# Optimization experiments

Measured on AMD Instinct MI355X. Metric: run time of the kernel, lower is better.

Reference implementation:

```python
import jax, jax.numpy as jnp
import numpy as np

NH, KD, VD, C = 8, 64, 64, 256

def conv1x1(x, w, b):
    # x: (B,C,D,H,W), w: (O,C), b: (O,)
    return jnp.einsum('bcdhw,oc->bodhw', x, w) + b[None, :, None, None, None]

def setup_inputs() -> dict:
    key = jax.random.key(0)
    ks = jax.random.split(key, 8)
    B, D, H, W = 2, 32, 32, 32
    s = 0.02
    return {
        'x': jax.random.normal(ks[0], (B, C, D, H, W), jnp.float32),
        'q_w': jax.random.normal(ks[1], (NH * KD, C), jnp.float32) * s,
        'q_b': jnp.zeros((NH * KD,), jnp.float32),
        'kv_w': jax.random.normal(ks[2], (KD + VD, C), jnp.float32) * s,
        'kv_b': jnp.zeros((KD + VD,), jnp.float32),
        'proj_w': jax.random.normal(ks[3], (C, NH * VD), jnp.float32) * s,
        'proj_b': jnp.zeros((C,), jnp.float32),
        'layer_scale': jnp.full((C, 1, 1, 1), 1e-5, jnp.float32),
    }

def reference(x, q_w, q_b, kv_w, kv_b, proj_w, proj_b, layer_scale):
    B, Cc, D, H, W = x.shape
    scale = VD ** -0.5
    # q: (B, nh, D, H, W, kd) -> flatten(3,5) -> (B, nh, D, H*W*kd)
    q = conv1x1(x, q_w, q_b).reshape(B, NH, KD, D, H, W).transpose(0, 1, 3, 4, 5, 2)
    q = q.reshape(B, NH, D, H * W * KD)
    kv = conv1x1(x, kv_w, kv_b)  # (B, kd+vd, D, H, W)
    k = kv[:, :KD].transpose(0, 2, 3, 4, 1).reshape(B, D, H * W * KD)  # shared across heads
    v = kv[:, KD:].transpose(0, 2, 3, 4, 1).reshape(B, D, H * W * VD)
    attn = jax.nn.softmax(jnp.einsum('bnqf,bkf->bnqk', q, k) * scale, axis=-1)  # (B,nh,D,D)
    o = jnp.einsum('bnqk,bkf->bnqf', attn, v)  # (B, nh, D, H*W*vd)
    # transpose(1,2) then row-major reshape, exactly as torch
    o = o.transpose(0, 2, 1, 3).reshape(B, D, H, W, NH * VD).transpose(0, 4, 1, 2, 3)
    out = conv1x1(o, proj_w, proj_b)
    return out * layer_scale[None]
```

## Files before the change

### kernel.cpp

```cpp
#include <hip/hip_runtime.h>
#include <math.h>

#define SS 32768
#define FQL_LDS_BYTES 149504

typedef _Float16 half4v __attribute__((ext_vector_type(4)));
typedef _Float16 half8v __attribute__((ext_vector_type(8)));
typedef float float4v __attribute__((ext_vector_type(4)));

__device__ __forceinline__ void gload16(const void* g, void* l) {
    __builtin_amdgcn_global_load_lds(
        (const __attribute__((address_space(1))) unsigned int*)g,
        (__attribute__((address_space(3))) unsigned int*)l, 16, 0, 0);
}

__global__ __launch_bounds__(256)
void cvt_x_kernel(const float* __restrict__ x, _Float16* __restrict__ x_t)
{
    __shared__ float ls[64][65];
    const int b = blockIdx.z, c0 = blockIdx.y * 64, s0 = blockIdx.x * 64;
    const int t = threadIdx.x;
    const int tr = t >> 4, tc = t & 15;
#pragma unroll
    for (int p = 0; p < 4; p++) {
        int c_l = p * 16 + tr;
        float4v v = *(const float4v*)(x + (size_t)(b * 256 + c0 + c_l) * SS + s0 + tc * 4);
        ls[c_l][tc * 4 + 0] = v.x;
        ls[c_l][tc * 4 + 1] = v.y;
        ls[c_l][tc * 4 + 2] = v.z;
        ls[c_l][tc * 4 + 3] = v.w;
    }
    __syncthreads();
#pragma unroll
    for (int p = 0; p < 4; p++) {
        int s_l = p * 16 + tr;
        half4v h;
        h.x = (_Float16)ls[tc * 4 + 0][s_l];
        h.y = (_Float16)ls[tc * 4 + 1][s_l];
        h.z = (_Float16)ls[tc * 4 + 2][s_l];
        h.w = (_Float16)ls[tc * 4 + 3][s_l];
        *(half4v*)(x_t + ((size_t)b * SS + s0 + s_l) * 256 + c0 + tc * 4) = h;
    }
}

__global__ __launch_bounds__(256)
void cvt_w3_kernel(const float* __restrict__ s0, _Float16* __restrict__ d0,
                   const float* __restrict__ s1, _Float16* __restrict__ d1,
                   const float* __restrict__ s2, _Float16* __restrict__ d2)
{
    int bx = blockIdx.x;
    if (bx < 128) {
        int idx = (bx * 256 + threadIdx.x) * 4;
        int e = idx & 7;
        int lane = (idx >> 3) & 63;
        int l15 = lane & 15, lq = lane >> 4;
        int blk = idx >> 9;
        int i = blk & 3, ks = (blk >> 2) & 7, nh = blk >> 5;
        const float* src = s0 + (size_t)(nh * 64 + i * 16 + l15) * 256 + ks * 32 + lq * 8 + e;
        float4v v = *(const float4v*)src;
        half4v hh;
        hh.x = (_Float16)v.x; hh.y = (_Float16)v.y; hh.z = (_Float16)v.z; hh.w = (_Float16)v.w;
        *(half4v*)(d0 + idx) = hh;
    } else {
        const float* s; _Float16* d; int base;
        if (bx < 160) { s = s1; d = d1; base = bx - 128; }
        else          { s = s2; d = d2; base = bx - 160; }
        int i = (base * 256 + threadIdx.x) * 4;
        float4v v = *(const float4v*)(s + i);
        half4v hh;
        hh.x = (_Float16)v.x; hh.y = (_Float16)v.y; hh.z = (_Float16)v.z; hh.w = (_Float16)v.w;
        *(half4v*)(d + i) = hh;
    }
}

__global__ __launch_bounds__(256)
void convkv_kernel(const _Float16* __restrict__ x_t,
                   const _Float16* __restrict__ wkv,
                   const float* __restrict__ kv_b,
                   _Float16* __restrict__ kv_t)
{
    __shared__ _Float16 smem[128 * 136];
    _Float16* const Ws = smem;
    _Float16* const Xs = smem + 128 * 64;
    const int b = blockIdx.y;
    const int s0 = blockIdx.x * 128;
    const int t = threadIdx.x;
    const int w = t >> 6, l = t & 63;
    const int om = (w & 1) * 64, sn = (w >> 1) * 64;

    const int lr = l >> 3;
    const int gch = ((l & 7) - lr) & 7;
    const int m15 = l & 15;
    const int sl0 = ((((l >> 4) + (l & 7)) & 7)) * 8;
    const int sl1 = ((((l >> 4) + 4 + (l & 7)) & 7)) * 8;

    float4v acc[4][4];
#pragma unroll
    for (int i = 0; i < 4; i++)
#pragma unroll
        for (int j = 0; j < 4; j++) acc[i][j] = (float4v){0.f, 0.f, 0.f, 0.f};

    const _Float16* wg = wkv + (size_t)(32 * w + lr) * 256 + gch * 8;
    const _Float16* xg = x_t + ((size_t)b * SS + s0 + 32 * w + lr) * 256 + gch * 8;
    _Float16* wl = &Ws[(32 * w) * 64];
    _Float16* xl = &Xs[(32 * w) * 64];

    for (int c0 = 0; c0 < 256; c0 += 64) {
#pragma unroll
        for (int rb = 0; rb < 4; rb++) {
            gload16(wg + (size_t)rb * 8 * 256 + c0, wl + rb * 8 * 64);
            gload16(xg + (size_t)rb * 8 * 256 + c0, xl + rb * 8 * 64);
        }
        __syncthreads();
#pragma unroll
        for (int ks = 0; ks < 2; ks++) {
            const int sl = ks ? sl1 : sl0;
            half8v a[4], bb[4];
#pragma unroll
            for (int i = 0; i < 4; i++)
                a[i] = *(const half8v*)&Ws[(om + i * 16 + m15) * 64 + sl];
#pragma unroll
            for (int j = 0; j < 4; j++)
                bb[j] = *(const half8v*)&Xs[(sn + j * 16 + m15) * 64 + sl];
#pragma unroll
            for (int i = 0; i < 4; i++)
#pragma unroll
                for (int j = 0; j < 4; j++)
                    acc[i][j] = __builtin_amdgcn_mfma_f32_16x16x32_f16(a[i], bb[j], acc[i][j], 0, 0, 0);
        }
        __syncthreads();
    }
    const int qd = l >> 4, m = l & 15;
#pragma unroll
    for (int i = 0; i < 4; i++) {
        float bv[4];
#pragma unroll
        for (int r = 0; r < 4; r++) bv[r] = kv_b[om + i * 16 + qd * 4 + r];
#pragma unroll
        for (int j = 0; j < 4; j++) {
            half4v h;
            h.x = (_Float16)(acc[i][j].x + bv[0]);
            h.y = (_Float16)(acc[i][j].y + bv[1]);
            h.z = (_Float16)(acc[i][j].z + bv[2]);
            h.w = (_Float16)(acc[i][j].w + bv[3]);
            int s_l = sn + j * 16 + m;
            *(half4v*)&smem[s_l * 136 + om + i * 16 + qd * 4] = h;
        }
    }
    __syncthreads();
    const int sr = t >> 4, kk = t & 15;
#pragma unroll
    for (int p = 0; p < 8; p++) {
        int s_l = p * 16 + sr;
        half8v h8 = *(const half8v*)&smem[s_l * 136 + kk * 8];
        *(half8v*)(kv_t + ((size_t)b * SS + s0 + s_l) * 128 + kk * 8) = h8;
    }
}

__global__ __launch_bounds__(512)
void fq_logits_kernel(const _Float16* __restrict__ x_t,
                      const _Float16* __restrict__ wq_f,
                      const float* __restrict__ q_b,
                      const _Float16* __restrict__ kv_t,
                      float* __restrict__ Lpart)
{
    extern __shared__ _Float16 sm[];
    _Float16* const Xs = sm;
    _Float16* const Qs = sm + 32768;
    float* const scr = (float*)(sm + 65536);

    const int chunk = blockIdx.x, b = blockIdx.y;
    const int hw0 = chunk * 4;
    const int t = threadIdx.x;
    const int w = t >> 6, l = t & 63;
    const int l15 = l & 15, lq = l >> 4;
    const int h = w >> 1;
    const int ns = w & 1;
    const int n0 = ns * 64;

#pragma unroll
    for (int ii = 0; ii < 8; ii++) {
        int r = w * 16 + ii * 2 + (l >> 5);
        int p = l & 31;
        int sc = (p - 4 * r) & 31;
        int qd = r >> 2, hwl = r & 3;
        gload16(x_t + ((size_t)b * SS + qd * 1024 + hw0 + hwl) * 256 + sc * 8,
                Xs + (w * 16 + ii * 2) * 256);
    }

    half8v bk[8];
#pragma unroll
    for (int j = 0; j < 2; j++)
#pragma unroll
        for (int ksp = 0; ksp < 4; ksp++) {
            int kk = (ns * 4 + ksp) * 32 + lq * 8;
            bk[j * 4 + ksp] = *(const half8v*)(kv_t +
                ((size_t)b * SS + (size_t)(j * 16 + l15) * 1024 + hw0 + (kk >> 6)) * 128 + (kk & 63));
        }
    __syncthreads();

    _Float16* const Qs_h = Qs + h * 8192;
    float* const scr_h = scr + h * (32 * 36);
    float* const lp_g = Lpart + (((size_t)chunk * 2 + b) * 8) * 1024;

    for (int g = 0; g < 2; g++) {
        const int nh = g * 4 + h;
        const _Float16* wf = wq_f + ((size_t)nh * 32) * 512 + (size_t)l * 8;
        half8v aF[4], aN[4];
#pragma unroll
        for (int i = 0; i < 4; i++) aF[i] = *(const half8v*)(wf + (size_t)i * 512);
        float4v acc[4][4];
#pragma unroll
        for (int i = 0; i < 4; i++)
#pragma unroll
            for (int j = 0; j < 4; j++) acc[i][j] = (float4v){0.f, 0.f, 0.f, 0.f};
#pragma unroll
        for (int ks = 0; ks < 8; ks++) {
            if (ks < 7) {
#pragma unroll
                for (int i = 0; i < 4; i++)
                    aN[i] = *(const half8v*)(wf + (size_t)((ks + 1) * 4 + i) * 512);
            }
            const int p8 = (((ks * 4 + lq) + 4 * (l15 & 7)) & 31) * 8;
            half8v bF[4];
#pragma unroll
            for (int j = 0; j < 4; j++)
                bF[j] = *(const half8v*)&Xs[(n0 + j * 16 + l15) * 256 + p8];
#pragma unroll
            for (int i = 0; i < 4; i++)
#pragma unroll
                for (int j = 0; j < 4; j++)
                    acc[i][j] = __builtin_amdgcn_mfma_f32_16x16x32_f16(aF[i], bF[j], acc[i][j], 0, 0, 0);
#pragma unroll
            for (int i = 0; i < 4; i++) aF[i] = aN[i];
        }
#pragma unroll
        for (int i = 0; i < 4; i++) {
            int kb = i * 16 + lq * 4;
            float4v bv = *(const float4v*)(q_b + nh * 64 + kb);
#pragma unroll
            for (int j = 0; j < 4; j++) {
                int sp = n0 + j * 16 + l15;
                int key = ((sp ^ (sp >> 2)) & 7) << 3;
                half4v hv;
                hv.x = (_Float16)(acc[i][j].x + bv.x);
                hv.y = (_Float16)(acc[i][j].y + bv.y);
                hv.z = (_Float16)(acc[i][j].z + bv.z);
                hv.w = (_Float16)(acc[i][j].w + bv.w);
                *(half4v*)&Qs_h[sp * 64 + (kb ^ key)] = hv;
            }
        }
        __syncthreads();
        float4v lacc[2][2];
#pragma unroll
        for (int i = 0; i < 2; i++)
#pragma unroll
            for (int j = 0; j < 2; j++) lacc[i][j] = (float4v){0.f, 0.f, 0.f, 0.f};
#pragma unroll
        for (int ksp = 0; ksp < 4; ksp++) {
            int kk = (ns * 4 + ksp) * 32 + lq * 8;
            half8v a0, a1;
            {
                int sp = l15 * 4 + (kk >> 6);
                int key = ((sp ^ (sp >> 2)) & 7) << 3;
                a0 = *(const half8v*)&Qs_h[sp * 64 + ((kk & 63) ^ key)];
            }
            {
                int sp = (16 + l15) * 4 + (kk >> 6);
                int key = ((sp ^ (sp >> 2)) & 7) << 3;
                a1 = *(const half8v*)&Qs_h[sp * 64 + ((kk & 63) ^ key)];
            }
            lacc[0][0] = __builtin_amdgcn_mfma_f32_16x16x32_f16(a0, bk[ksp],     lacc[0][0], 0, 0, 0);
            lacc[0][1] = __builtin_amdgcn_mfma_f32_16x16x32_f16(a0, bk[4 + ksp], lacc[0][1], 0, 0, 0);
            lacc[1][0] = __builtin_amdgcn_mfma_f32_16x16x32_f16(a1, bk[ksp],     lacc[1][0], 0, 0, 0);
            lacc[1][1] = __builtin_amdgcn_mfma_f32_16x16x32_f16(a1, bk[4 + ksp], lacc[1][1], 0, 0, 0);
        }
        if (ns == 1) {
#pragma unroll
            for (int i = 0; i < 2; i++)
#pragma unroll
                for (int j = 0; j < 2; j++)
                    *(float4v*)&scr_h[(j * 16 + l15) * 36 + i * 16 + lq * 4] = lacc[i][j];
        }
        __syncthreads();
        if (ns == 0) {
            float* dst = lp_g + (size_t)nh * 1024;
#pragma unroll
            for (int i = 0; i < 2; i++)
#pragma unroll
                for (int j = 0; j < 2; j++) {
                    float4v o = lacc[i][j];
                    float4v p4 = *(const float4v*)&scr_h[(j * 16 + l15) * 36 + i * 16 + lq * 4];
                    o += p4;
                    int rb = i * 16 + lq * 4;
#pragma unroll
                    for (int rr = 0; rr < 4; rr++)
                        dst[(rb + rr) * 32 + j * 16 + l15] = o[rr];
                }
        }
    }
}

__global__ __launch_bounds__(256)
void softmax_kernel(const float* __restrict__ Lpart, float* __restrict__ Lsm)
{
    __shared__ float red[32][8][32];
    const int t = threadIdx.x;
    const int rl = t & 7, cs = t >> 3;
    const int row = blockIdx.x * 8 + rl;
    const int b = row >> 8, nh = (row >> 5) & 7, qd = row & 31;
    float4v p[8];
#pragma unroll
    for (int j4 = 0; j4 < 8; j4++) p[j4] = (float4v){0.f, 0.f, 0.f, 0.f};
    for (int cc = 0; cc < 8; cc++) {
        int chunk = cs + cc * 32;
        const float* src = Lpart + (((size_t)chunk * 2 + b) * 8 + nh) * 1024 + qd * 32;
#pragma unroll
        for (int j4 = 0; j4 < 8; j4++) p[j4] += *(const float4v*)(src + j4 * 4);
    }
#pragma unroll
    for (int j4 = 0; j4 < 8; j4++) *(float4v*)&red[cs][rl][j4 * 4] = p[j4];
    __syncthreads();
    const int r2 = t >> 5, j = t & 31;
    float s = 0.f;
#pragma unroll
    for (int c2 = 0; c2 < 32; c2++) s += red[c2][r2][j];
    float mx = s;
#pragma unroll
    for (int off = 16; off >= 1; off >>= 1) mx = fmaxf(mx, __shfl_xor(mx, off, 32));
    float e = expf((s - mx) * 0.125f);
    float sum = e;
#pragma unroll
    for (int off = 16; off >= 1; off >>= 1) sum += __shfl_xor(sum, off, 32);
    Lsm[(size_t)(blockIdx.x * 8 + r2) * 32 + j] = e / sum;
}

__global__ __launch_bounds__(256)
void attn_v_kernel(const _Float16* __restrict__ kv_t,
                   const float* __restrict__ attn,
                   _Float16* __restrict__ o_t)
{
    __shared__ float as_[2048];
    const int wq = blockIdx.x, hl = blockIdx.y;
    const int b = blockIdx.z >> 2, rc = blockIdx.z & 3;
    const int t = threadIdx.x;
    {
        const float* src = attn + (size_t)b * 8192 + rc * 2048;
#pragma unroll
        for (int ll = 0; ll < 2; ll++) {
            int idx = (t + ll * 256) * 4;
            *(float4v*)(&as_[idx]) = *(const float4v*)(src + idx);
        }
    }
    __syncthreads();
    const int q4 = t & 127;
    const int half = t >> 7;
    const int tt = q4 >> 4;
    const int vd = (q4 * 4) & 63;
    const int hw = hl * 256 + wq * 8 + tt;
    float4v vreg[32];
#pragma unroll
    for (int j = 0; j < 32; j++) {
        half4v hv = *(const half4v*)(kv_t + ((size_t)((b * 32 + j) * 1024 + hw)) * 128 + 64 + vd);
        vreg[j] = (float4v){(float)hv.x, (float)hv.y, (float)hv.z, (float)hv.w};
    }
    _Float16* outb = o_t + (size_t)b * SS * 512;
#pragma unroll 2
    for (int rr = 0; rr < 32; rr++) {
        int row_l = half * 32 + rr;
        int row = rc * 64 + row_l;
        int hh = row >> 5, d = row & 31;
        const float* arow = &as_[row_l * 32];
        float ax = 0.f, ay = 0.f, az = 0.f, aw = 0.f;
#pragma unroll
        for (int j4 = 0; j4 < 8; j4++) {
            float4v a4 = *(const float4v*)(&arow[j4 * 4]);
            float4v v0 = vreg[j4 * 4 + 0];
            float4v v1 = vreg[j4 * 4 + 1];
            float4v v2 = vreg[j4 * 4 + 2];
            float4v v3 = vreg[j4 * 4 + 3];
            ax = fmaf(a4.x, v0.x, ax); ay = fmaf(a4.x, v0.y, ay);
            az = fmaf(a4.x, v0.z, az); aw = fmaf(a4.x, v0.w, aw);
            ax = fmaf(a4.y, v1.x, ax); ay = fmaf(a4.y, v1.y, ay);
            az = fmaf(a4.y, v1.z, az); aw = fmaf(a4.y, v1.w, aw);
            ax = fmaf(a4.z, v2.x, ax); ay = fmaf(a4.z, v2.y, ay);
            az = fmaf(a4.z, v2.z, az); aw = fmaf(a4.z, v2.w, aw);
            ax = fmaf(a4.w, v3.x, ax); ay = fmaf(a4.w, v3.y, ay);
            az = fmaf(a4.w, v3.z, az); aw = fmaf(a4.w, v3.w, aw);
        }
        int hp = hh * 4 + hl;
        size_t sp = (size_t)d * 1024 + hp * 32 + wq;
        half4v o4;
        o4.x = (_Float16)ax; o4.y = (_Float16)ay; o4.z = (_Float16)az; o4.w = (_Float16)aw;
        *(half4v*)(outb + sp * 512 + q4 * 4) = o4;
    }
}

__global__ __launch_bounds__(256)
void proj_mfma_kernel(const _Float16* __restrict__ o_t,
                      const _Float16* __restrict__ wp,
                      const float* __restrict__ pb,
                      const float* __restrict__ ls,
                      float* __restrict__ out)
{
    __shared__ _Float16 Ws[128 * 64];
    __shared__ _Float16 Xs[128 * 64];
    const int b = blockIdx.y;
    const int bx = blockIdx.x;
    const int grp = bx >> 4, rem = bx & 15;
    const int s_tile = grp * 8 + (rem & 7);
    const int o_tile = rem >> 3;
    const int s0 = s_tile * 128, o0 = o_tile * 128;
    const int t = threadIdx.x;
    const int w = t >> 6, l = t & 63;
    const int om = (w & 1) * 64, sn = (w >> 1) * 64;

    const int lr = l >> 3;
    const int gch = ((l & 7) - lr) & 7;
    const int m15 = l & 15;
    const int sl0 = ((((l >> 4) + (l & 7)) & 7)) * 8;
    const int sl1 = ((((l >> 4) + 4 + (l & 7)) & 7)) * 8;

    float4v acc[4][4];
#pragma unroll
    for (int i = 0; i < 4; i++)
#pragma unroll
        for (int j = 0; j < 4; j++) acc[i][j] = (float4v){0.f, 0.f, 0.f, 0.f};

    const _Float16* wg = wp + (size_t)(o0 + 32 * w + lr) * 512 + gch * 8;
    const _Float16* xg = o_t + ((size_t)b * SS + s0 + 32 * w + lr) * 512 + gch * 8;
    _Float16* wl = &Ws[(32 * w) * 64];
    _Float16* xl = &Xs[(32 * w) * 64];

    for (int c0 = 0; c0 < 512; c0 += 64) {
#pragma unroll
        for (int rb = 0; rb < 4; rb++) {
            gload16(wg + (size_t)rb * 8 * 512 + c0, wl + rb * 8 * 64);
            gload16(xg + (size_t)rb * 8 * 512 + c0, xl + rb * 8 * 64);
        }
        __syncthreads();
#pragma unroll
        for (int ks = 0; ks < 2; ks++) {
            const int sl = ks ? sl1 : sl0;
            half8v a[4], bb[4];
#pragma unroll
            for (int i = 0; i < 4; i++)
                a[i] = *(const half8v*)&Ws[(om + i * 16 + m15) * 64 + sl];
#pragma unroll
            for (int j = 0; j < 4; j++)
                bb[j] = *(const half8v*)&Xs[(sn + j * 16 + m15) * 64 + sl];
#pragma unroll
            for (int i = 0; i < 4; i++)
#pragma unroll
                for (int j = 0; j < 4; j++)
                    acc[i][j] = __builtin_amdgcn_mfma_f32_16x16x32_f16(a[i], bb[j], acc[i][j], 0, 0, 0);
        }
        __syncthreads();
    }
    const int qd = l >> 4, m = l & 15;
#pragma unroll
    for (int i = 0; i < 4; i++) {
        float pbv[4], lsv[4];
#pragma unroll
        for (int r = 0; r < 4; r++) {
            int o = o0 + om + i * 16 + qd * 4 + r;
            pbv[r] = pb[o];
            lsv[r] = ls[o];
        }
#pragma unroll
        for (int j = 0; j < 4; j++) {
            int s = s0 + sn + j * 16 + m;
#pragma unroll
            for (int r = 0; r < 4; r++) {
                int o = o0 + om + i * 16 + qd * 4 + r;
                out[((size_t)b * 256 + o) * SS + s] = (acc[i][j][r] + pbv[r]) * lsv[r];
            }
        }
    }
}

extern "C" void kernel_launch(void* const* d_in, const int* in_sizes, int n_in,
                              void* d_out, int out_size, void* d_ws, size_t ws_size,
                              hipStream_t stream)
{
    const float* x      = (const float*)d_in[0];
    const float* q_w    = (const float*)d_in[1];
    const float* q_b    = (const float*)d_in[2];
    const float* kv_w   = (const float*)d_in[3];
    const float* kv_b   = (const float*)d_in[4];
    const float* proj_w = (const float*)d_in[5];
    const float* proj_b = (const float*)d_in[6];
    const float* ls     = (const float*)d_in[7];
    float* out = (float*)d_out;

    char* ws = (char*)d_ws;
    _Float16* x_t  = (_Float16*)(ws);
    _Float16* o_t  = (_Float16*)(ws + 33554432);
    float*    Lpart= (float*)   (ws + 33554432);
    _Float16* kv_t = (_Float16*)(ws + 100663296);
    float*    Lsm  = (float*)   (ws + 117440512);
    _Float16* wq_f = (_Float16*)(ws + 117506048);
    _Float16* wkv  = (_Float16*)(ws + 117768192);
    _Float16* wp   = (_Float16*)(ws + 117833728);

    static bool fql_attr_set = false;
    if (!fql_attr_set) {
        hipFuncSetAttribute(reinterpret_cast<const void*>(fq_logits_kernel),
                            hipFuncAttributeMaxDynamicSharedMemorySize, FQL_LDS_BYTES);
        fql_attr_set = true;
    }

    cvt_x_kernel<<<dim3(512, 4, 2), 256, 0, stream>>>(x, x_t);
    cvt_w3_kernel<<<dim3(288), 256, 0, stream>>>(q_w, wq_f, kv_w, wkv, proj_w, wp);

    convkv_kernel<<<dim3(256, 2), 256, 0, stream>>>(x_t, wkv, kv_b, kv_t);
    fq_logits_kernel<<<dim3(256, 2), 512, FQL_LDS_BYTES, stream>>>(x_t, wq_f, q_b, kv_t, Lpart);
    softmax_kernel<<<dim3(64), 256, 0, stream>>>(Lpart, Lsm);
    attn_v_kernel<<<dim3(32, 4, 8), 256, 0, stream>>>(kv_t, Lsm, o_t);
    proj_mfma_kernel<<<dim3(512, 2), 256, 0, stream>>>(o_t, wp, proj_b, ls, out);
}
```

Measured before the change: 242.1 us.

## Fuse KV 1x1 conv into fused Q-logits kernel, computing K/V from LDS-resident x tile

Removes the separate convkv kernel. The fq_logits kernel now computes K and V for its own 128 spatial positions from the x tile already in LDS, keeps K in LDS for the logits and writes only V to global memory for the attn_v stage. The weight conversion for kv_w moves to the fragment-packed layout used for q_w. The logits reduction is reorganised so each wave covers all 256 K-steps for half the rows, which drops the cross-wave scratch reduction. In exchange the fused kernel does more work per block and needs an extra sync and LDS region reuse.

```diff
diff --git a/kernel.cpp b/kernel.cpp
--- a/kernel.cpp
+++ b/kernel.cpp
@@ -2,7 +2,7 @@
 #include <math.h>
 
 #define SS 32768
-#define FQL_LDS_BYTES 149504
+#define FQL_LDS_BYTES 147456
 
 typedef _Float16 half4v __attribute__((ext_vector_type(4)));
 typedef _Float16 half8v __attribute__((ext_vector_type(8)));
@@ -49,111 +49,27 @@
                    const float* __restrict__ s2, _Float16* __restrict__ d2)
 {
     int bx = blockIdx.x;
-    if (bx < 128) {
-        int idx = (bx * 256 + threadIdx.x) * 4;
+    if (bx < 160) {
+        const float* s; _Float16* d; int base;
+        if (bx < 128) { s = s0; d = d0; base = bx; }
+        else          { s = s1; d = d1; base = bx - 128; }
+        int idx = (base * 256 + threadIdx.x) * 4;
         int e = idx & 7;
         int lane = (idx >> 3) & 63;
         int l15 = lane & 15, lq = lane >> 4;
         int blk = idx >> 9;
-        int i = blk & 3, ks = (blk >> 2) & 7, nh = blk >> 5;
-        const float* src = s0 + (size_t)(nh * 64 + i * 16 + l15) * 256 + ks * 32 + lq * 8 + e;
+        int i = blk & 3, ks = (blk >> 2) & 7, slab = blk >> 5;
+        const float* src = s + (size_t)(slab * 64 + i * 16 + l15) * 256 + ks * 32 + lq * 8 + e;
         float4v v = *(const float4v*)src;
         half4v hh;
         hh.x = (_Float16)v.x; hh.y = (_Float16)v.y; hh.z = (_Float16)v.z; hh.w = (_Float16)v.w;
-        *(half4v*)(d0 + idx) = hh;
+        *(half4v*)(d + idx) = hh;
     } else {
-        const float* s; _Float16* d; int base;
-        if (bx < 160) { s = s1; d = d1; base = bx - 128; }
-        else          { s = s2; d = d2; base = bx - 160; }
-        int i = (base * 256 + threadIdx.x) * 4;
-        float4v v = *(const float4v*)(s + i);
+        int i = ((bx - 160) * 256 + threadIdx.x) * 4;
+        float4v v = *(const float4v*)(s2 + i);
         half4v hh;
         hh.x = (_Float16)v.x; hh.y = (_Float16)v.y; hh.z = (_Float16)v.z; hh.w = (_Float16)v.w;
-        *(half4v*)(d + i) = hh;
-    }
-}
-
-__global__ __launch_bounds__(256)
-void convkv_kernel(const _Float16* __restrict__ x_t,
-                   const _Float16* __restrict__ wkv,
-                   const float* __restrict__ kv_b,
-                   _Float16* __restrict__ kv_t)
-{
-    __shared__ _Float16 smem[128 * 136];
-    _Float16* const Ws = smem;
-    _Float16* const Xs = smem + 128 * 64;
-    const int b = blockIdx.y;
-    const int s0 = blockIdx.x * 128;
-    const int t = threadIdx.x;
-    const int w = t >> 6, l = t & 63;
-    const int om = (w & 1) * 64, sn = (w >> 1) * 64;
-
-    const int lr = l >> 3;
-    const int gch = ((l & 7) - lr) & 7;
-    const int m15 = l & 15;
-    const int sl0 = ((((l >> 4) + (l & 7)) & 7)) * 8;
-    const int sl1 = ((((l >> 4) + 4 + (l & 7)) & 7)) * 8;
-
-    float4v acc[4][4];
-#pragma unroll
-    for (int i = 0; i < 4; i++)
-#pragma unroll
-        for (int j = 0; j < 4; j++) acc[i][j] = (float4v){0.f, 0.f, 0.f, 0.f};
-
-    const _Float16* wg = wkv + (size_t)(32 * w + lr) * 256 + gch * 8;
-    const _Float16* xg = x_t + ((size_t)b * SS + s0 + 32 * w + lr) * 256 + gch * 8;
-    _Float16* wl = &Ws[(32 * w) * 64];
-    _Float16* xl = &Xs[(32 * w) * 64];
-
-    for (int c0 = 0; c0 < 256; c0 += 64) {
-#pragma unroll
-        for (int rb = 0; rb < 4; rb++) {
-            gload16(wg + (size_t)rb * 8 * 256 + c0, wl + rb * 8 * 64);
-            gload16(xg + (size_t)rb * 8 * 256 + c0, xl + rb * 8 * 64);
-        }
-        __syncthreads();
-#pragma unroll
-        for (int ks = 0; ks < 2; ks++) {
-            const int sl = ks ? sl1 : sl0;
-            half8v a[4], bb[4];
-#pragma unroll
-            for (int i = 0; i < 4; i++)
-                a[i] = *(const half8v*)&Ws[(om + i * 16 + m15) * 64 + sl];
-#pragma unroll
-            for (int j = 0; j < 4; j++)
-                bb[j] = *(const half8v*)&Xs[(sn + j * 16 + m15) * 64 + sl];
-#pragma unroll
-            for (int i = 0; i < 4; i++)
-#pragma unroll
-                for (int j = 0; j < 4; j++)
-                    acc[i][j] = __builtin_amdgcn_mfma_f32_16x16x32_f16(a[i], bb[j], acc[i][j], 0, 0, 0);
-        }
-        __syncthreads();
-    }
-    const int qd = l >> 4, m = l & 15;
-#pragma unroll
-    for (int i = 0; i < 4; i++) {
-        float bv[4];
-#pragma unroll
-        for (int r = 0; r < 4; r++) bv[r] = kv_b[om + i * 16 + qd * 4 + r];
-#pragma unroll
-        for (int j = 0; j < 4; j++) {
-            half4v h;
-            h.x = (_Float16)(acc[i][j].x + bv[0]);
-            h.y = (_Float16)(acc[i][j].y + bv[1]);
-            h.z = (_Float16)(acc[i][j].z + bv[2]);
-            h.w = (_Float16)(acc[i][j].w + bv[3]);
-            int s_l = sn + j * 16 + m;
-            *(half4v*)&smem[s_l * 136 + om + i * 16 + qd * 4] = h;
-        }
-    }
-    __syncthreads();
-    const int sr = t >> 4, kk = t & 15;
-#pragma unroll
-    for (int p = 0; p < 8; p++) {
-        int s_l = p * 16 + sr;
-        half8v h8 = *(const half8v*)&smem[s_l * 136 + kk * 8];
-        *(half8v*)(kv_t + ((size_t)b * SS + s0 + s_l) * 128 + kk * 8) = h8;
+        *(half4v*)(d2 + i) = hh;
     }
 }
 
@@ -161,22 +77,22 @@
 void fq_logits_kernel(const _Float16* __restrict__ x_t,
                       const _Float16* __restrict__ wq_f,
                       const float* __restrict__ q_b,
-                      const _Float16* __restrict__ kv_t,
+                      const _Float16* __restrict__ wkv_f,
+                      const float* __restrict__ kv_b,
+                      _Float16* __restrict__ kv_t,
                       float* __restrict__ Lpart)
 {
     extern __shared__ _Float16 sm[];
-    _Float16* const Xs = sm;
-    _Float16* const Qs = sm + 32768;
-    float* const scr = (float*)(sm + 65536);
+    _Float16* const Xs  = sm;
+    _Float16* const Qs  = sm + 32768;
+    _Float16* const Vst = sm + 32768;
+    _Float16* const Ks  = sm + 65536;
 
     const int chunk = blockIdx.x, b = blockIdx.y;
     const int hw0 = chunk * 4;
     const int t = threadIdx.x;
     const int w = t >> 6, l = t & 63;
     const int l15 = l & 15, lq = l >> 4;
-    const int h = w >> 1;
-    const int ns = w & 1;
-    const int n0 = ns * 64;
 
 #pragma unroll
     for (int ii = 0; ii < 8; ii++) {
@@ -187,20 +103,75 @@
         gload16(x_t + ((size_t)b * SS + qd * 1024 + hw0 + hwl) * 256 + sc * 8,
                 Xs + (w * 16 + ii * 2) * 256);
     }
-
-    half8v bk[8];
-#pragma unroll
-    for (int j = 0; j < 2; j++)
-#pragma unroll
-        for (int ksp = 0; ksp < 4; ksp++) {
-            int kk = (ns * 4 + ksp) * 32 + lq * 8;
-            bk[j * 4 + ksp] = *(const half8v*)(kv_t +
-                ((size_t)b * SS + (size_t)(j * 16 + l15) * 1024 + hw0 + (kk >> 6)) * 128 + (kk & 63));
-        }
-    __syncthreads();
-
+    __syncthreads();
+
+    {
+        const int slab = w & 1, nq = w >> 1;
+        const int n0k = nq * 32;
+        const _Float16* wf = wkv_f + ((size_t)slab * 32) * 512 + (size_t)l * 8;
+        half8v aF[4], aN[4];
+#pragma unroll
+        for (int i = 0; i < 4; i++) aF[i] = *(const half8v*)(wf + (size_t)i * 512);
+        float4v acc[4][2];
+#pragma unroll
+        for (int i = 0; i < 4; i++)
+#pragma unroll
+            for (int j = 0; j < 2; j++) acc[i][j] = (float4v){0.f, 0.f, 0.f, 0.f};
+#pragma unroll
+        for (int ks = 0; ks < 8; ks++) {
+            if (ks < 7) {
+#pragma unroll
+                for (int i = 0; i < 4; i++)
+                    aN[i] = *(const half8v*)(wf + (size_t)((ks + 1) * 4 + i) * 512);
+            }
+            const int p8 = (((ks * 4 + lq) + 4 * (l15 & 7)) & 31) * 8;
+            half8v bF[2];
+#pragma unroll
+            for (int j = 0; j < 2; j++)
+                bF[j] = *(const half8v*)&Xs[(n0k + j * 16 + l15) * 256 + p8];
+#pragma unroll
+            for (int i = 0; i < 4; i++)
+#pragma unroll
+                for (int j = 0; j < 2; j++)
+                    acc[i][j] = __builtin_amdgcn_mfma_f32_16x16x32_f16(aF[i], bF[j], acc[i][j], 0, 0, 0);
+#pragma unroll
+            for (int i = 0; i < 4; i++) aF[i] = aN[i];
+        }
+#pragma unroll
+        for (int i = 0; i < 4; i++) {
+            int kb = i * 16 + lq * 4;
+            float4v bv = *(const float4v*)(kv_b + slab * 64 + kb);
+#pragma unroll
+            for (int j = 0; j < 2; j++) {
+                int sp = n0k + j * 16 + l15;
+                int key = ((sp ^ (sp >> 2)) & 7) << 3;
+                half4v hv;
+                hv.x = (_Float16)(acc[i][j].x + bv.x);
+                hv.y = (_Float16)(acc[i][j].y + bv.y);
+                hv.z = (_Float16)(acc[i][j].z + bv.z);
+                hv.w = (_Float16)(acc[i][j].w + bv.w);
+                if (slab == 0) *(half4v*)&Ks[sp * 64 + (kb ^ key)] = hv;
+                else           *(half4v*)&Vst[sp * 64 + (kb ^ key)] = hv;
+            }
+        }
+    }
+    __syncthreads();
+
+#pragma unroll
+    for (int p = 0; p < 2; p++) {
+        int sp_l = (t >> 3) + p * 64;
+        int c0 = (t & 7) * 8;
+        int key = ((sp_l ^ (sp_l >> 2)) & 7) << 3;
+        half8v h8 = *(const half8v*)&Vst[sp_l * 64 + (c0 ^ key)];
+        int qd = sp_l >> 2, hwl = sp_l & 3;
+        *(half8v*)(kv_t + ((size_t)b * SS + qd * 1024 + hw0 + hwl) * 128 + 64 + c0) = h8;
+    }
+    __syncthreads();
+
+    const int h = w >> 1;
+    const int rh = w & 1;
+    const int n0 = rh * 64;
     _Float16* const Qs_h = Qs + h * 8192;
-    float* const scr_h = scr + h * (32 * 36);
     float* const lp_g = Lpart + (((size_t)chunk * 2 + b) * 8) * 1024;
 
     for (int g = 0; g < 2; g++) {
@@ -251,53 +222,39 @@
             }
         }
         __syncthreads();
-        float4v lacc[2][2];
-#pragma unroll
-        for (int i = 0; i < 2; i++)
-#pragma unroll
-            for (int j = 0; j < 2; j++) lacc[i][j] = (float4v){0.f, 0.f, 0.f, 0.f};
-#pragma unroll
-        for (int ksp = 0; ksp < 4; ksp++) {
-            int kk = (ns * 4 + ksp) * 32 + lq * 8;
-            half8v a0, a1;
+        float4v lacc[2];
+        lacc[0] = (float4v){0.f, 0.f, 0.f, 0.f};
+        lacc[1] = (float4v){0.f, 0.f, 0.f, 0.f};
+#pragma unroll
+        for (int ks = 0; ks < 8; ks++) {
+            int kk = ks * 32 + lq * 8;
+            int hwl = kk >> 6, kc = kk & 63;
+            half8v a, b0, b1;
             {
-                int sp = l15 * 4 + (kk >> 6);
+                int sp = (rh * 16 + l15) * 4 + hwl;
                 int key = ((sp ^ (sp >> 2)) & 7) << 3;
-                a0 = *(const half8v*)&Qs_h[sp * 64 + ((kk & 63) ^ key)];
+                a = *(const half8v*)&Qs_h[sp * 64 + (kc ^ key)];
             }
             {
-                int sp = (16 + l15) * 4 + (kk >> 6);
+                int sp = l15 * 4 + hwl;
                 int key = ((sp ^ (sp >> 2)) & 7) << 3;
-                a1 = *(const half8v*)&Qs_h[sp * 64 + ((kk & 63) ^ key)];
-            }
-            lacc[0][0] = __builtin_amdgcn_mfma_f32_16x16x32_f16(a0, bk[ksp],     lacc[0][0], 0, 0, 0);
-            lacc[0][1] = __builtin_amdgcn_mfma_f32_16x16x32_f16(a0, bk[4 + ksp], lacc[0][1], 0, 0, 0);
-            lacc[1][0] = __builtin_amdgcn_mfma_f32_16x16x32_f16(a1, bk[ksp],     lacc[1][0], 0, 0, 0);
-            lacc[1][1] = __builtin_amdgcn_mfma_f32_16x16x32_f16(a1, bk[4 + ksp], lacc[1][1], 0, 0, 0);
-        }
-        if (ns == 1) {
-#pragma unroll
-            for (int i = 0; i < 2; i++)
-#pragma unroll
-                for (int j = 0; j < 2; j++)
-                    *(float4v*)&scr_h[(j * 16 + l15) * 36 + i * 16 + lq * 4] = lacc[i][j];
-        }
+                b0 = *(const half8v*)&Ks[sp * 64 + (kc ^ key)];
+            }
+            {
+                int sp = (16 + l15) * 4 + hwl;
+                int key = ((sp ^ (sp >> 2)) & 7) << 3;
+                b1 = *(const half8v*)&Ks[sp * 64 + (kc ^ key)];
+            }
+            lacc[0] = __builtin_amdgcn_mfma_f32_16x16x32_f16(a, b0, lacc[0], 0, 0, 0);
+            lacc[1] = __builtin_amdgcn_mfma_f32_16x16x32_f16(a, b1, lacc[1], 0, 0, 0);
+        }
+        float* dst = lp_g + (size_t)nh * 1024;
+#pragma unroll
+        for (int jt = 0; jt < 2; jt++)
+#pragma unroll
+            for (int rr = 0; rr < 4; rr++)
+                dst[(rh * 16 + lq * 4 + rr) * 32 + jt * 16 + l15] = lacc[jt][rr];
         __syncthreads();
-        if (ns == 0) {
-            float* dst = lp_g + (size_t)nh * 1024;
-#pragma unroll
-            for (int i = 0; i < 2; i++)
-#pragma unroll
-                for (int j = 0; j < 2; j++) {
-                    float4v o = lacc[i][j];
-                    float4v p4 = *(const float4v*)&scr_h[(j * 16 + l15) * 36 + i * 16 + lq * 4];
-                    o += p4;
-                    int rb = i * 16 + lq * 4;
-#pragma unroll
-                    for (int rr = 0; rr < 4; rr++)
-                        dst[(rb + rr) * 32 + j * 16 + l15] = o[rr];
-                }
-        }
     }
 }
 
@@ -500,7 +457,7 @@
     _Float16* kv_t = (_Float16*)(ws + 100663296);
     float*    Lsm  = (float*)   (ws + 117440512);
     _Float16* wq_f = (_Float16*)(ws + 117506048);
-    _Float16* wkv  = (_Float16*)(ws + 117768192);
+    _Float16* wkv_f= (_Float16*)(ws + 117768192);
     _Float16* wp   = (_Float16*)(ws + 117833728);
 
     static bool fql_attr_set = false;
@@ -511,10 +468,10 @@
     }
 
     cvt_x_kernel<<<dim3(512, 4, 2), 256, 0, stream>>>(x, x_t);
-    cvt_w3_kernel<<<dim3(288), 256, 0, stream>>>(q_w, wq_f, kv_w, wkv, proj_w, wp);
-
-    convkv_kernel<<<dim3(256, 2), 256, 0, stream>>>(x_t, wkv, kv_b, kv_t);
-    fq_logits_kernel<<<dim3(256, 2), 512, FQL_LDS_BYTES, stream>>>(x_t, wq_f, q_b, kv_t, Lpart);
+    cvt_w3_kernel<<<dim3(288), 256, 0, stream>>>(q_w, wq_f, kv_w, wkv_f, proj_w, wp);
+
+    fq_logits_kernel<<<dim3(256, 2), 512, FQL_LDS_BYTES, stream>>>(
+        x_t, wq_f, q_b, wkv_f, kv_b, kv_t, Lpart);
     softmax_kernel<<<dim3(64), 256, 0, stream>>>(Lpart, Lsm);
     attn_v_kernel<<<dim3(32, 4, 8), 256, 0, stream>>>(kv_t, Lsm, o_t);
     proj_mfma_kernel<<<dim3(512, 2), 256, 0, stream>>>(o_t, wp, proj_b, ls, out);
```

Result: no change. 246.6 us (+1.9%).

## Pre-swizzle projection weights into MFMA fragment layout and compute all outputs per block

Applied to the files above, without the earlier changes.

The proj weight is converted into an MFMA-fragment-ordered fp16 layout so each lane can load its A operands straight from global memory (L2-resident), with no staging through LDS. Each proj block now covers all 256 output channels for a 128-spatial tile, so the o_t activation tile is read once instead of twice, and the grid halves. This doubles the accumulator count per thread (128 floats), which raises register pressure and may lower occupancy, and it adds global-load latency inside the inner loop.

```diff
diff --git a/kernel.cpp b/kernel.cpp
--- a/kernel.cpp
+++ b/kernel.cpp
@@ -61,15 +61,24 @@
         half4v hh;
         hh.x = (_Float16)v.x; hh.y = (_Float16)v.y; hh.z = (_Float16)v.z; hh.w = (_Float16)v.w;
         *(half4v*)(d0 + idx) = hh;
-    } else {
-        const float* s; _Float16* d; int base;
-        if (bx < 160) { s = s1; d = d1; base = bx - 128; }
-        else          { s = s2; d = d2; base = bx - 160; }
-        int i = (base * 256 + threadIdx.x) * 4;
-        float4v v = *(const float4v*)(s + i);
+    } else if (bx < 160) {
+        int i = ((bx - 128) * 256 + threadIdx.x) * 4;
+        float4v v = *(const float4v*)(s1 + i);
         half4v hh;
         hh.x = (_Float16)v.x; hh.y = (_Float16)v.y; hh.z = (_Float16)v.z; hh.w = (_Float16)v.w;
-        *(half4v*)(d + i) = hh;
+        *(half4v*)(d1 + i) = hh;
+    } else {
+        int idx = ((bx - 160) * 256 + threadIdx.x) * 4;
+        int e = idx & 7;
+        int lane = (idx >> 3) & 63;
+        int l15 = lane & 15, lq = lane >> 4;
+        int blk = idx >> 9;
+        int i = blk & 15, ks = blk >> 4;
+        const float* src = s2 + (size_t)(i * 16 + l15) * 512 + ks * 32 + lq * 8 + e;
+        float4v v = *(const float4v*)src;
+        half4v hh;
+        hh.x = (_Float16)v.x; hh.y = (_Float16)v.y; hh.z = (_Float16)v.z; hh.w = (_Float16)v.w;
+        *(half4v*)(d2 + idx) = hh;
     }
 }
 
@@ -398,81 +407,71 @@
 
 __global__ __launch_bounds__(256)
 void proj_mfma_kernel(const _Float16* __restrict__ o_t,
-                      const _Float16* __restrict__ wp,
+                      const _Float16* __restrict__ wp_f,
                       const float* __restrict__ pb,
                       const float* __restrict__ ls,
                       float* __restrict__ out)
 {
-    __shared__ _Float16 Ws[128 * 64];
     __shared__ _Float16 Xs[128 * 64];
     const int b = blockIdx.y;
-    const int bx = blockIdx.x;
-    const int grp = bx >> 4, rem = bx & 15;
-    const int s_tile = grp * 8 + (rem & 7);
-    const int o_tile = rem >> 3;
-    const int s0 = s_tile * 128, o0 = o_tile * 128;
+    const int s0 = blockIdx.x * 128;
     const int t = threadIdx.x;
     const int w = t >> 6, l = t & 63;
-    const int om = (w & 1) * 64, sn = (w >> 1) * 64;
+    const int l15 = l & 15, lq = l >> 4;
 
     const int lr = l >> 3;
     const int gch = ((l & 7) - lr) & 7;
-    const int m15 = l & 15;
-    const int sl0 = ((((l >> 4) + (l & 7)) & 7)) * 8;
-    const int sl1 = ((((l >> 4) + 4 + (l & 7)) & 7)) * 8;
-
-    float4v acc[4][4];
+    const int sl0 = ((lq + (l & 7)) & 7) * 8;
+    const int sl1 = ((lq + 4 + (l & 7)) & 7) * 8;
+
+    float4v acc[4][8];
 #pragma unroll
     for (int i = 0; i < 4; i++)
 #pragma unroll
-        for (int j = 0; j < 4; j++) acc[i][j] = (float4v){0.f, 0.f, 0.f, 0.f};
-
-    const _Float16* wg = wp + (size_t)(o0 + 32 * w + lr) * 512 + gch * 8;
+        for (int j = 0; j < 8; j++) acc[i][j] = (float4v){0.f, 0.f, 0.f, 0.f};
+
     const _Float16* xg = o_t + ((size_t)b * SS + s0 + 32 * w + lr) * 512 + gch * 8;
-    _Float16* wl = &Ws[(32 * w) * 64];
     _Float16* xl = &Xs[(32 * w) * 64];
+    const _Float16* wf = wp_f + (size_t)l * 8;
 
     for (int c0 = 0; c0 < 512; c0 += 64) {
 #pragma unroll
-        for (int rb = 0; rb < 4; rb++) {
-            gload16(wg + (size_t)rb * 8 * 512 + c0, wl + rb * 8 * 64);
+        for (int rb = 0; rb < 4; rb++)
             gload16(xg + (size_t)rb * 8 * 512 + c0, xl + rb * 8 * 64);
-        }
         __syncthreads();
 #pragma unroll
         for (int ks = 0; ks < 2; ks++) {
             const int sl = ks ? sl1 : sl0;
-            half8v a[4], bb[4];
+            half8v a[4], bb[8];
 #pragma unroll
             for (int i = 0; i < 4; i++)
-                a[i] = *(const half8v*)&Ws[(om + i * 16 + m15) * 64 + sl];
-#pragma unroll
-            for (int j = 0; j < 4; j++)
-                bb[j] = *(const half8v*)&Xs[(sn + j * 16 + m15) * 64 + sl];
+                a[i] = *(const half8v*)(wf + (size_t)(((c0 >> 5) + ks) * 16 + w * 4 + i) * 512);
+#pragma unroll
+            for (int j = 0; j < 8; j++)
+                bb[j] = *(const half8v*)&Xs[(j * 16 + l15) * 64 + sl];
 #pragma unroll
             for (int i = 0; i < 4; i++)
 #pragma unroll
-                for (int j = 0; j < 4; j++)
+                for (int j = 0; j < 8; j++)
                     acc[i][j] = __builtin_amdgcn_mfma_f32_16x16x32_f16(a[i], bb[j], acc[i][j], 0, 0, 0);
         }
         __syncthreads();
     }
-    const int qd = l >> 4, m = l & 15;
 #pragma unroll
     for (int i = 0; i < 4; i++) {
         float pbv[4], lsv[4];
 #pragma unroll
         for (int r = 0; r < 4; r++) {
-            int o = o0 + om + i * 16 + qd * 4 + r;
+            int o = w * 64 + i * 16 + lq * 4 + r;
             pbv[r] = pb[o];
             lsv[r] = ls[o];
         }
 #pragma unroll
-        for (int j = 0; j < 4; j++) {
-            int s = s0 + sn + j * 16 + m;
+        for (int j = 0; j < 8; j++) {
+            int s = s0 + j * 16 + l15;
 #pragma unroll
             for (int r = 0; r < 4; r++) {
-                int o = o0 + om + i * 16 + qd * 4 + r;
+                int o = w * 64 + i * 16 + lq * 4 + r;
                 out[((size_t)b * 256 + o) * SS + s] = (acc[i][j][r] + pbv[r]) * lsv[r];
             }
         }
@@ -501,7 +500,7 @@
     float*    Lsm  = (float*)   (ws + 117440512);
     _Float16* wq_f = (_Float16*)(ws + 117506048);
     _Float16* wkv  = (_Float16*)(ws + 117768192);
-    _Float16* wp   = (_Float16*)(ws + 117833728);
+    _Float16* wp_f = (_Float16*)(ws + 117833728);
 
     static bool fql_attr_set = false;
     if (!fql_attr_set) {
@@ -511,11 +510,12 @@
     }
 
     cvt_x_kernel<<<dim3(512, 4, 2), 256, 0, stream>>>(x, x_t);
-    cvt_w3_kernel<<<dim3(288), 256, 0, stream>>>(q_w, wq_f, kv_w, wkv, proj_w, wp);
+    cvt_w3_kernel<<<dim3(288), 256, 0, stream>>>(q_w, wq_f, kv_w, wkv, proj_w, wp_f);
 
     convkv_kernel<<<dim3(256, 2), 256, 0, stream>>>(x_t, wkv, kv_b, kv_t);
-    fq_logits_kernel<<<dim3(256, 2), 512, FQL_LDS_BYTES, stream>>>(x_t, wq_f, q_b, kv_t, Lpart);
+    fq_logits_kernel<<<dim3(256, 2), 512, FQL_LDS_BYTES, stream>>>(
+        x_t, wq_f, q_b, kv_t, Lpart);
     softmax_kernel<<<dim3(64), 256, 0, stream>>>(Lpart, Lsm);
     attn_v_kernel<<<dim3(32, 4, 8), 256, 0, stream>>>(kv_t, Lsm, o_t);
-    proj_mfma_kernel<<<dim3(512, 2), 256, 0, stream>>>(o_t, wp, proj_b, ls, out);
-}
+    proj_mfma_kernel<<<dim3(256, 2), 256, 0, stream>>>(o_t, wp_f, proj_b, ls, out);
+}
```

Result: slower. 257.6 us (+6.4%).
